# Performance work log

Measured on AMD Instinct MI355X. Metric: run time of the kernel, lower is better.

## Reference

```python
import jax, jax.numpy as jnp
import numpy as np

N, NIN, NOUT = 8192, 512, 512


def setup_inputs() -> dict:
    key = jax.random.key(0)
    k1, k2, k3 = jax.random.split(key, 3)
    H = jax.random.normal(k1, (N, NIN), dtype=jnp.float32)
    adj_matrix = jax.random.uniform(k2, (N, N), dtype=jnp.float32)
    W = jax.random.normal(k3, (NOUT, NIN), dtype=jnp.float32) / np.sqrt(NIN)
    b = jnp.zeros((NOUT,), dtype=jnp.float32)
    return {"H": H, "adj_matrix": adj_matrix, "W": W, "b": b}


def reference(H, adj_matrix, W, b):
    n = adj_matrix.shape[0]
    # adj + I (self-loops)
    A = adj_matrix + jnp.eye(n, dtype=adj_matrix.dtype)
    # column degrees (torch.sum(dim=0))
    deg = jnp.sum(A, axis=0)
    d = deg ** -0.5
    d = jnp.where(jnp.isinf(d), 0.0, d)
    # D^-1/2 A D^-1/2 implemented as elementwise row/col rescale (same math as diag matmuls)
    A = d[:, None] * A * d[None, :]
    # message passing + linear (torch Linear: x @ W.T + b) + tanh
    Hm = A @ H  # [N, nin]
    out = jnp.tanh(Hm @ W.T + b)
    return out
```

## Files before the change

### kernel.cpp

```cpp
#include <hip/hip_runtime.h>
#include <hip/hip_bf16.h>

#define N_NODES 8192
#define N_IN 512
#define N_OUT 512

typedef __bf16 bf16;
typedef __bf16 bf16x4 __attribute__((ext_vector_type(4)));
typedef __bf16 bf16x8 __attribute__((ext_vector_type(8)));
typedef float f32x4 __attribute__((ext_vector_type(4)));

__device__ __forceinline__ void gload16(const void* g, void* l) {
  __builtin_amdgcn_global_load_lds((const __attribute__((address_space(1))) void*)g,
                                   (__attribute__((address_space(3))) void*)l, 16, 0, 0);
}

#define WAITVM(N) asm volatile("s_waitcnt vmcnt(" #N ")" ::: "memory")
#define BAR() do { asm volatile("" ::: "memory"); __builtin_amdgcn_s_barrier(); \
                   asm volatile("" ::: "memory"); } while (0)

__global__ __launch_bounds__(256) void k_colsum_cvt(const float* __restrict__ adj,
                                                    bf16* __restrict__ adjb,
                                                    float* __restrict__ partial) {
  const int tid  = threadIdx.x;
  const int col0 = blockIdx.x * 1024 + tid * 4;
  const int row0 = blockIdx.y * 64;
  float s0 = 0.f, s1 = 0.f, s2 = 0.f, s3 = 0.f;
#pragma unroll 4
  for (int r = 0; r < 64; ++r) {
    float4 v = *reinterpret_cast<const float4*>(adj + (size_t)(row0 + r) * N_NODES + col0);
    s0 += v.x; s1 += v.y; s2 += v.z; s3 += v.w;
    const int dq = row0 + r - col0;
    if ((unsigned)dq < 4u) reinterpret_cast<float*>(&v)[dq] += 1.0f;
    bf16x4 o = { (bf16)v.x, (bf16)v.y, (bf16)v.z, (bf16)v.w };
    *reinterpret_cast<bf16x4*>(adjb + (size_t)(row0 + r) * N_NODES + col0) = o;
  }
  float4 ps = { s0, s1, s2, s3 };
  *reinterpret_cast<float4*>(partial + (size_t)blockIdx.y * N_NODES + col0) = ps;
}

__global__ __launch_bounds__(256) void k_dvec(const float* __restrict__ partial,
                                              float* __restrict__ dv) {
  const int j = blockIdx.x * 256 + threadIdx.x;
  float s = 1.0f;
#pragma unroll 8
  for (int p = 0; p < 128; ++p) s += partial[(size_t)p * N_NODES + j];
  dv[j] = rsqrtf(s);
}

__global__ __launch_bounds__(256) void k_hst(const float* __restrict__ H,
                                             const float* __restrict__ dv,
                                             bf16* __restrict__ Hst) {
  __shared__ float t[64][65];
  const int tid = threadIdx.x;
  const int j0 = blockIdx.x * 64;
  const int k0 = blockIdx.y * 64;
  const int rr = tid >> 4;
  const int cc = (tid & 15) * 4;
#pragma unroll
  for (int p = 0; p < 4; ++p) {
    const int r = p * 16 + rr;
    const float d = dv[j0 + r];
    float4 v = *reinterpret_cast<const float4*>(H + (size_t)(j0 + r) * N_IN + k0 + cc);
    t[r][cc + 0] = v.x * d; t[r][cc + 1] = v.y * d;
    t[r][cc + 2] = v.z * d; t[r][cc + 3] = v.w * d;
  }
  __syncthreads();
#pragma unroll
  for (int p = 0; p < 4; ++p) {
    const int kr = p * 16 + rr;
    bf16x4 o = { (bf16)t[cc + 0][kr], (bf16)t[cc + 1][kr],
                 (bf16)t[cc + 2][kr], (bf16)t[cc + 3][kr] };
    *reinterpret_cast<bf16x4*>(Hst + (size_t)(k0 + kr) * N_NODES + j0 + cc) = o;
  }
}

__global__ __launch_bounds__(256) void k_wcvt(const float* __restrict__ W, bf16* __restrict__ Wb) {
  const int i = (blockIdx.x * 256 + threadIdx.x) * 4;
  float4 v = *reinterpret_cast<const float4*>(W + i);
  bf16x4 o = { (bf16)v.x, (bf16)v.y, (bf16)v.z, (bf16)v.w };
  *reinterpret_cast<bf16x4*>(Wb + i) = o;
}

template<int KDIM, int NSPLIT>
__global__ __launch_bounds__(512, 2) void k_gemm256(
    const bf16* __restrict__ A, const bf16* __restrict__ B, float* __restrict__ P) {
  constexpr int KSEG = KDIM / NSPLIT;
  constexpr int NT = KSEG / 32;
  constexpr int NTN = 2;
  constexpr int NBLK = 32 * NTN * NSPLIT;
  __shared__ __attribute__((aligned(128))) char lds[4 * 32768];

  const int bid = blockIdx.x;
  const int logical = (bid & 7) * (NBLK / 8) + (bid >> 3);
  const int split = logical / (32 * NTN);
  const int rem = logical % (32 * NTN);
  const int bm0 = (rem >> 1) * 256;
  const int bn0 = (rem & 1) * 256;

  const int tid = threadIdx.x;
  const int lane = tid & 63;
  const int wid = tid >> 6;
  const int wr = wid >> 2;
  const int wc = wid & 3;

  const int srow = tid >> 2;
  const int scol = ((tid & 3) ^ ((srow >> 1) & 3)) << 3;
  const size_t a_src = (size_t)(bm0 + srow) * KDIM + (size_t)split * KSEG + scol;
  const size_t b_src = (size_t)(bn0 + srow) * KDIM + (size_t)split * KSEG + scol;

  const int frow = lane & 15;
  const int fk = lane >> 4;
  const int colb = (fk << 4) ^ (((frow >> 1) & 3) << 4);
  const int a_base = (wr * 128 + frow) * 64 + colb;
  const int b_base = 16384 + (wc * 64 + frow) * 64 + colb;

  f32x4 acc[8][4] = {};

  auto stage_full = [&](int t) {
    char* sb = lds + (t & 3) * 32768;
    const bf16* ag = A + a_src + (size_t)t * 32;
    const bf16* bg = B + b_src + (size_t)t * 32;
    gload16(ag,                      sb +         tid * 16);
    gload16(ag + (size_t)128 * KDIM, sb +  8192 + tid * 16);
    gload16(bg,                      sb + 16384 + tid * 16);
    gload16(bg + (size_t)128 * KDIM, sb + 24576 + tid * 16);
  };

  stage_full(0); stage_full(1);
  WAITVM(4);
  BAR();

#pragma unroll 1
  for (int t = 0; t < NT; ++t) {
    const char* lbase = lds + (t & 3) * 32768;
    char* sbase = lds + ((t + 2) & 3) * 32768;
    const bf16* ag = A + a_src + (size_t)(t + 2) * 32;
    const bf16* bg = B + b_src + (size_t)(t + 2) * 32;
    const bool pf = (t + 2 < NT);

    bf16x8 av[8], bv[4];
#pragma unroll
    for (int m = 0; m < 4; ++m)
      av[m] = *reinterpret_cast<const bf16x8*>(lbase + a_base + m * 1024);
#pragma unroll
    for (int n = 0; n < 4; ++n)
      bv[n] = *reinterpret_cast<const bf16x8*>(lbase + b_base + n * 1024);
    if (pf) {
      gload16(ag,                      sbase +        tid * 16);
      gload16(ag + (size_t)128 * KDIM, sbase + 8192 + tid * 16);
    }
    BAR();
    __builtin_amdgcn_s_setprio(1);
#pragma unroll
    for (int m = 0; m < 4; ++m)
#pragma unroll
      for (int n = 0; n < 4; ++n)
        acc[m][n] = __builtin_amdgcn_mfma_f32_16x16x32_bf16(av[m], bv[n], acc[m][n], 0, 0, 0);
    __builtin_amdgcn_s_setprio(0);
    BAR();
#pragma unroll
    for (int m = 4; m < 8; ++m)
      av[m] = *reinterpret_cast<const bf16x8*>(lbase + a_base + m * 1024);
    if (pf) {
      gload16(bg,                      sbase + 16384 + tid * 16);
      gload16(bg + (size_t)128 * KDIM, sbase + 24576 + tid * 16);
    }
    BAR();
    __builtin_amdgcn_s_setprio(1);
#pragma unroll
    for (int m = 4; m < 8; ++m)
#pragma unroll
      for (int n = 0; n < 4; ++n)
        acc[m][n] = __builtin_amdgcn_mfma_f32_16x16x32_bf16(av[m], bv[n], acc[m][n], 0, 0, 0);
    __builtin_amdgcn_s_setprio(0);
    if (pf) WAITVM(4); else WAITVM(0);
    BAR();
  }

#pragma unroll
  for (int m = 0; m < 8; ++m) {
#pragma unroll
    for (int j = 0; j < 4; ++j) {
      const int grow = bm0 + wr * 128 + m * 16 + (lane >> 4) * 4 + j;
      float* prow = P + (size_t)split * ((size_t)N_NODES * N_IN) + (size_t)grow * N_IN;
#pragma unroll
      for (int n = 0; n < 4; ++n) {
        const int gcol = bn0 + wc * 64 + n * 16 + (lane & 15);
        prow[gcol] = acc[m][n][j];
      }
    }
  }
}

template<int KDIM>
__global__ __launch_bounds__(256, 2) void k_gemm(
    const bf16* __restrict__ A, const bf16* __restrict__ B,
    const float* __restrict__ bias, float* __restrict__ outf) {
  constexpr int NT = KDIM / 64;
  constexpr int NBLK = 256;
  __shared__ __attribute__((aligned(128))) char lds[2 * 32768];

  const int bid = blockIdx.x;
  const int logical = (bid & 7) * (NBLK / 8) + (bid >> 3);
  const int bm0 = (logical >> 2) * 128;
  const int bn0 = (logical & 3) * 128;

  const int tid = threadIdx.x;
  const int wid = tid >> 6;
  const int lane = tid & 63;
  const int wr = wid & 1, wc = wid >> 1;

  const int srow = tid >> 3;
  const int scol = ((tid & 7) ^ (srow & 7)) << 3;
  const size_t a_src = (size_t)(bm0 + srow) * KDIM + scol;
  const size_t b_src = (size_t)(bn0 + srow) * KDIM + scol;

  const int frow = lane & 15;
  const int fk = lane >> 4;
  const int swz = (lane & 7) << 4;
  const int a_row_byte = (wr * 64 + frow) * 128;
  const int b_row_byte = 16384 + (wc * 64 + frow) * 128;

  f32x4 acc[4][4] = {};

  auto stage = [&](int t) {
    char* lbase = lds + (t & 1) * 32768;
    const bf16* ag = A + a_src + (size_t)t * 64;
    const bf16* bg = B + b_src + (size_t)t * 64;
#pragma unroll
    for (int ch = 0; ch < 4; ++ch) {
      gload16(ag + (size_t)(ch * 32) * KDIM, lbase + ch * 4096 + wid * 1024);
      gload16(bg + (size_t)(ch * 32) * KDIM, lbase + 16384 + ch * 4096 + wid * 1024);
    }
  };

  auto compute = [&](int t) {
    const char* lbase = lds + (t & 1) * 32768;
#pragma unroll
    for (int kk = 0; kk < 2; ++kk) {
      const int colb = (kk * 64 + fk * 16) ^ swz;
      bf16x8 av[4], bv[4];
#pragma unroll
      for (int m = 0; m < 4; ++m)
        av[m] = *reinterpret_cast<const bf16x8*>(lbase + a_row_byte + m * 2048 + colb);
#pragma unroll
      for (int n = 0; n < 4; ++n)
        bv[n] = *reinterpret_cast<const bf16x8*>(lbase + b_row_byte + n * 2048 + colb);
#pragma unroll
      for (int m = 0; m < 4; ++m)
#pragma unroll
        for (int n = 0; n < 4; ++n)
          acc[m][n] = __builtin_amdgcn_mfma_f32_16x16x32_bf16(av[m], bv[n], acc[m][n], 0, 0, 0);
    }
  };

  stage(0);
#pragma unroll 1
  for (int t = 0; t < NT - 1; ++t) {
    stage(t + 1);
    WAITVM(8);
    BAR();
    compute(t);
    BAR();
  }
  WAITVM(0);
  BAR();
  compute(NT - 1);

#pragma unroll
  for (int m = 0; m < 4; ++m) {
#pragma unroll
    for (int j = 0; j < 4; ++j) {
      const int grow = bm0 + wr * 64 + m * 16 + (lane >> 4) * 4 + j;
      float* orow = outf + (size_t)grow * N_OUT;
#pragma unroll
      for (int n = 0; n < 4; ++n) {
        const int gcol = bn0 + wc * 64 + n * 16 + (lane & 15);
        float v = acc[m][n][j] + bias[gcol];
        v = fminf(fmaxf(v, -15.f), 15.f);
        const float e = __expf(2.f * v);
        orow[gcol] = (e - 1.f) / (e + 1.f);
      }
    }
  }
}

__global__ __launch_bounds__(256) void k_red(const float* __restrict__ P,
                                             const float* __restrict__ dv,
                                             bf16* __restrict__ Hm) {
  const int t = blockIdx.x * 256 + threadIdx.x;
  const int row = t >> 7;
  const int col = (t & 127) << 2;
  const size_t off = (size_t)row * N_IN + col;
  constexpr size_t S = (size_t)N_NODES * N_IN;
  const float d = dv[row];
  const float4 p0 = *reinterpret_cast<const float4*>(P + off);
  const float4 p1 = *reinterpret_cast<const float4*>(P + S + off);
  const float4 p2 = *reinterpret_cast<const float4*>(P + 2 * S + off);
  const float4 p3 = *reinterpret_cast<const float4*>(P + 3 * S + off);
  bf16x4 o = { (bf16)(d * ((p0.x + p1.x) + (p2.x + p3.x))),
               (bf16)(d * ((p0.y + p1.y) + (p2.y + p3.y))),
               (bf16)(d * ((p0.z + p1.z) + (p2.z + p3.z))),
               (bf16)(d * ((p0.w + p1.w) + (p2.w + p3.w))) };
  *reinterpret_cast<bf16x4*>(Hm + off) = o;
}

extern "C" void kernel_launch(void* const* d_in, const int* in_sizes, int n_in,
                              void* d_out, int out_size, void* d_ws, size_t ws_size,
                              hipStream_t stream) {
  const float* H   = (const float*)d_in[0];
  const float* adj = (const float*)d_in[1];
  const float* W   = (const float*)d_in[2];
  const float* b   = (const float*)d_in[3];
  float* out = (float*)d_out;
  char* ws = (char*)d_ws;

  bf16*  adjb = (bf16*)(ws);
  bf16*  Hst  = (bf16*)(ws + 134217728);
  bf16*  Hm   = (bf16*)(ws + 142606336);
  bf16*  Wb   = (bf16*)(ws + 150994944);
  float* part = (float*)(ws + 151519232);
  float* dv   = (float*)(ws + 155713536);
  float* P    = (float*)(ws + 155746304);

  k_colsum_cvt<<<dim3(8, 128), 256, 0, stream>>>(adj, adjb, part);
  k_dvec<<<32, 256, 0, stream>>>(part, dv);
  k_hst<<<dim3(128, 8), 256, 0, stream>>>(H, dv, Hst);
  k_wcvt<<<256, 256, 0, stream>>>(W, Wb);
  k_gemm256<8192, 4><<<256, 512, 0, stream>>>(adjb, Hst, P);
  k_red<<<4096, 256, 0, stream>>>(P, dv, Hm);
  k_gemm<512><<<256, 256, 0, stream>>>(Hm, Wb, b, out);
}
```

Baseline: 212.2 us.

## Deepen K-tile to 64 with four-phase interleaved prefetch in 256x256 GEMM

Restructures the 256x256 bf16 MFMA GEMM main loop to process K in 64-wide tiles with two 64KB LDS buffers instead of four 32-wide buffers. Each tile is split into four MFMA phases with global-to-LDS loads for the next tiles spread across them and fine-grained vmcnt waits. It also switches to an 8-way XOR swizzle over 128-byte rows. The aim is fewer barrier-bound iterations and better overlap of loads with MFMA work. In exchange there are more barriers per iteration, more complex wait counts, and B fragments held in registers across phases.

```diff
diff --git a/kernel.cpp b/kernel.cpp
--- a/kernel.cpp
+++ b/kernel.cpp
@@ -86,10 +86,10 @@
 __global__ __launch_bounds__(512, 2) void k_gemm256(
     const bf16* __restrict__ A, const bf16* __restrict__ B, float* __restrict__ P) {
   constexpr int KSEG = KDIM / NSPLIT;
-  constexpr int NT = KSEG / 32;
+  constexpr int NT = KSEG / 64;
   constexpr int NTN = 2;
   constexpr int NBLK = 32 * NTN * NSPLIT;
-  __shared__ __attribute__((aligned(128))) char lds[4 * 32768];
+  __shared__ __attribute__((aligned(128))) char lds[2 * 65536];
 
   const int bid = blockIdx.x;
   const int logical = (bid & 7) * (NBLK / 8) + (bid >> 3);
@@ -104,79 +104,105 @@
   const int wr = wid >> 2;
   const int wc = wid & 3;
 
-  const int srow = tid >> 2;
-  const int scol = ((tid & 3) ^ ((srow >> 1) & 3)) << 3;
-  const size_t a_src = (size_t)(bm0 + srow) * KDIM + (size_t)split * KSEG + scol;
-  const size_t b_src = (size_t)(bn0 + srow) * KDIM + (size_t)split * KSEG + scol;
+  const int lrow = lane >> 3;
+  const int g_srow = wid * 8 + lrow;
+  const int g_scol = ((lane & 7) ^ lrow) << 3;
+  const size_t koff = (size_t)split * KSEG;
+  const bf16* aP = A + (size_t)(bm0 + g_srow) * KDIM + koff + g_scol;
+  const bf16* bP = B + (size_t)(bn0 + g_srow) * KDIM + koff + g_scol;
+  const int ldst = wid * 1024;
 
   const int frow = lane & 15;
   const int fk = lane >> 4;
-  const int colb = (fk << 4) ^ (((frow >> 1) & 3) << 4);
-  const int a_base = (wr * 128 + frow) * 64 + colb;
-  const int b_base = 16384 + (wc * 64 + frow) * 64 + colb;
+  const int e7 = lane & 7;
+  const int sb0 = ((fk ^ e7) << 4);
+  const int sb1 = (((4 + fk) ^ e7) << 4);
+  const int a_b = (wr * 128 + frow) * 128;
+  const int b_b = 32768 + (wc * 64 + frow) * 128;
 
   f32x4 acc[8][4] = {};
 
-  auto stage_full = [&](int t) {
-    char* sb = lds + (t & 3) * 32768;
-    const bf16* ag = A + a_src + (size_t)t * 32;
-    const bf16* bg = B + b_src + (size_t)t * 32;
-    gload16(ag,                      sb +         tid * 16);
-    gload16(ag + (size_t)128 * KDIM, sb +  8192 + tid * 16);
-    gload16(bg,                      sb + 16384 + tid * 16);
-    gload16(bg + (size_t)128 * KDIM, sb + 24576 + tid * 16);
-  };
-
-  stage_full(0); stage_full(1);
-  WAITVM(4);
+  auto GLA = [&](int kt, int q, int buf) {
+    gload16(aP + (size_t)(q * 64) * KDIM + (size_t)kt * 64,
+            lds + buf * 65536 + q * 8192 + ldst);
+  };
+  auto GLB = [&](int kt, int q, int buf) {
+    gload16(bP + (size_t)(q * 64) * KDIM + (size_t)kt * 64,
+            lds + buf * 65536 + 32768 + q * 8192 + ldst);
+  };
+
+  auto phases = [&](int kt, bool s1, bool s2, bool s3, int f2, int f4) {
+    const char* lb = lds + (kt & 1) * 65536;
+    const int ob = (kt & 1) ^ 1;
+    const int cb = (kt & 1);
+    bf16x8 av[4], bv0[4], bv1[4];
+#pragma unroll
+    for (int m = 0; m < 4; ++m) av[m]  = *(const bf16x8*)(lb + a_b + m * 2048 + sb0);
+#pragma unroll
+    for (int n = 0; n < 4; ++n) bv0[n] = *(const bf16x8*)(lb + b_b + n * 2048 + sb0);
+#pragma unroll
+    for (int n = 0; n < 4; ++n) bv1[n] = *(const bf16x8*)(lb + b_b + n * 2048 + sb1);
+    if (s1) { GLA(kt + 1, 1, ob); GLA(kt + 1, 3, ob); }
+    BAR();
+    __builtin_amdgcn_s_setprio(1);
+#pragma unroll
+    for (int m = 0; m < 4; ++m)
+#pragma unroll
+      for (int n = 0; n < 4; ++n)
+        acc[m][n] = __builtin_amdgcn_mfma_f32_16x16x32_bf16(av[m], bv0[n], acc[m][n], 0, 0, 0);
+    __builtin_amdgcn_s_setprio(0);
+    BAR();
+#pragma unroll
+    for (int m = 0; m < 4; ++m) av[m] = *(const bf16x8*)(lb + a_b + m * 2048 + sb1);
+    if (s2) { GLB(kt + 2, 0, cb); GLB(kt + 2, 1, cb); }
+    BAR();
+    __builtin_amdgcn_s_setprio(1);
+#pragma unroll
+    for (int m = 0; m < 4; ++m)
+#pragma unroll
+      for (int n = 0; n < 4; ++n)
+        acc[m][n] = __builtin_amdgcn_mfma_f32_16x16x32_bf16(av[m], bv1[n], acc[m][n], 0, 0, 0);
+    __builtin_amdgcn_s_setprio(0);
+    if (f2 == 0) WAITVM(10); else if (f2 == 1) WAITVM(8); else WAITVM(0);
+    BAR();
+#pragma unroll
+    for (int m = 0; m < 4; ++m) av[m] = *(const bf16x8*)(lb + a_b + (m + 4) * 2048 + sb0);
+    if (s3) { GLB(kt + 2, 2, cb); GLB(kt + 2, 3, cb); GLA(kt + 2, 0, cb); GLA(kt + 2, 2, cb); }
+    BAR();
+    __builtin_amdgcn_s_setprio(1);
+#pragma unroll
+    for (int m = 0; m < 4; ++m)
+#pragma unroll
+      for (int n = 0; n < 4; ++n)
+        acc[m + 4][n] = __builtin_amdgcn_mfma_f32_16x16x32_bf16(av[m], bv0[n], acc[m + 4][n], 0, 0, 0);
+    __builtin_amdgcn_s_setprio(0);
+    BAR();
+#pragma unroll
+    for (int m = 0; m < 4; ++m) av[m] = *(const bf16x8*)(lb + a_b + (m + 4) * 2048 + sb1);
+    BAR();
+    __builtin_amdgcn_s_setprio(1);
+#pragma unroll
+    for (int m = 0; m < 4; ++m)
+#pragma unroll
+      for (int n = 0; n < 4; ++n)
+        acc[m + 4][n] = __builtin_amdgcn_mfma_f32_16x16x32_bf16(av[m], bv1[n], acc[m + 4][n], 0, 0, 0);
+    __builtin_amdgcn_s_setprio(0);
+    if (f4 == 0) WAITVM(8); else if (f4 == 1) WAITVM(2); else WAITVM(0);
+    BAR();
+  };
+
+  GLA(0, 0, 0); GLA(0, 2, 0); GLB(0, 0, 0); GLB(0, 1, 0); GLB(0, 2, 0); GLB(0, 3, 0);
+  GLA(0, 1, 0); GLA(0, 3, 0);
+  GLB(1, 0, 1); GLB(1, 1, 1);
+  GLB(1, 2, 1); GLB(1, 3, 1); GLA(1, 0, 1); GLA(1, 2, 1);
+  WAITVM(8);
   BAR();
 
 #pragma unroll 1
-  for (int t = 0; t < NT; ++t) {
-    const char* lbase = lds + (t & 3) * 32768;
-    char* sbase = lds + ((t + 2) & 3) * 32768;
-    const bf16* ag = A + a_src + (size_t)(t + 2) * 32;
-    const bf16* bg = B + b_src + (size_t)(t + 2) * 32;
-    const bool pf = (t + 2 < NT);
-
-    bf16x8 av[8], bv[4];
-#pragma unroll
-    for (int m = 0; m < 4; ++m)
-      av[m] = *reinterpret_cast<const bf16x8*>(lbase + a_base + m * 1024);
-#pragma unroll
-    for (int n = 0; n < 4; ++n)
-      bv[n] = *reinterpret_cast<const bf16x8*>(lbase + b_base + n * 1024);
-    if (pf) {
-      gload16(ag,                      sbase +        tid * 16);
-      gload16(ag + (size_t)128 * KDIM, sbase + 8192 + tid * 16);
-    }
-    BAR();
-    __builtin_amdgcn_s_setprio(1);
-#pragma unroll
-    for (int m = 0; m < 4; ++m)
-#pragma unroll
-      for (int n = 0; n < 4; ++n)
-        acc[m][n] = __builtin_amdgcn_mfma_f32_16x16x32_bf16(av[m], bv[n], acc[m][n], 0, 0, 0);
-    __builtin_amdgcn_s_setprio(0);
-    BAR();
-#pragma unroll
-    for (int m = 4; m < 8; ++m)
-      av[m] = *reinterpret_cast<const bf16x8*>(lbase + a_base + m * 1024);
-    if (pf) {
-      gload16(bg,                      sbase + 16384 + tid * 16);
-      gload16(bg + (size_t)128 * KDIM, sbase + 24576 + tid * 16);
-    }
-    BAR();
-    __builtin_amdgcn_s_setprio(1);
-#pragma unroll
-    for (int m = 4; m < 8; ++m)
-#pragma unroll
-      for (int n = 0; n < 4; ++n)
-        acc[m][n] = __builtin_amdgcn_mfma_f32_16x16x32_bf16(av[m], bv[n], acc[m][n], 0, 0, 0);
-    __builtin_amdgcn_s_setprio(0);
-    if (pf) WAITVM(4); else WAITVM(0);
-    BAR();
-  }
+  for (int kt = 0; kt < NT - 2; ++kt)
+    phases(kt, true, true, true, 0, 0);
+  phases(NT - 2, true, false, false, 1, 1);
+  phases(NT - 1, false, false, false, 2, 2);
 
 #pragma unroll
   for (int m = 0; m < 8; ++m) {
```

Result: faster. 206.6 us (-2.6%).

## Replace 256x256 pipelined GEMM with single-buffered 128x128 tile GEMM at higher occupancy

Applied to the files above, without the earlier changes.

The main adjacency GEMM moves from 256x256 tiles, 512 threads and a 4-stage LDS ring with software prefetch to 128x128 tiles, 256 threads and a single 32KB LDS buffer with K-steps of 64. It launches 1024 blocks instead of 256, relying on four blocks per CU to hide memory latency rather than explicit prefetch. The trade is lower data reuse per tile, which means more global traffic, plus full barriers with no load/compute overlap inside a block.

```diff
diff --git a/kernel.cpp b/kernel.cpp
--- a/kernel.cpp
+++ b/kernel.cpp
@@ -83,106 +83,79 @@
 }
 
 template<int KDIM, int NSPLIT>
-__global__ __launch_bounds__(512, 2) void k_gemm256(
+__global__ __launch_bounds__(256, 4) void k_gemm128(
     const bf16* __restrict__ A, const bf16* __restrict__ B, float* __restrict__ P) {
   constexpr int KSEG = KDIM / NSPLIT;
-  constexpr int NT = KSEG / 32;
-  constexpr int NTN = 2;
-  constexpr int NBLK = 32 * NTN * NSPLIT;
-  __shared__ __attribute__((aligned(128))) char lds[4 * 32768];
+  constexpr int NT = KSEG / 64;
+  constexpr int NBLK = 256 * NSPLIT;
+  __shared__ __attribute__((aligned(128))) char lds[32768];
 
   const int bid = blockIdx.x;
-  const int logical = (bid & 7) * (NBLK / 8) + (bid >> 3);
-  const int split = logical / (32 * NTN);
-  const int rem = logical % (32 * NTN);
-  const int bm0 = (rem >> 1) * 256;
-  const int bn0 = (rem & 1) * 256;
+  const int l = (bid & 7) * (NBLK / 8) + (bid >> 3);
+  const int split = l >> 8;
+  const int rem = l & 255;
+  const int bm0 = (rem >> 2) * 128;
+  const int bn0 = (rem & 3) * 128;
 
   const int tid = threadIdx.x;
   const int lane = tid & 63;
   const int wid = tid >> 6;
-  const int wr = wid >> 2;
-  const int wc = wid & 3;
-
-  const int srow = tid >> 2;
-  const int scol = ((tid & 3) ^ ((srow >> 1) & 3)) << 3;
-  const size_t a_src = (size_t)(bm0 + srow) * KDIM + (size_t)split * KSEG + scol;
-  const size_t b_src = (size_t)(bn0 + srow) * KDIM + (size_t)split * KSEG + scol;
+  const int wr = wid & 1, wc = wid >> 1;
+
+  const int srow = tid >> 3;
+  const int sslot = (tid & 7) ^ (srow & 7);
+  const size_t koff = (size_t)split * KSEG;
+  const bf16* aP = A + (size_t)(bm0 + srow) * KDIM + koff + sslot * 8;
+  const bf16* bP = B + (size_t)(bn0 + srow) * KDIM + koff + sslot * 8;
+  const int wuni = wid * 1024;
 
   const int frow = lane & 15;
   const int fk = lane >> 4;
-  const int colb = (fk << 4) ^ (((frow >> 1) & 3) << 4);
-  const int a_base = (wr * 128 + frow) * 64 + colb;
-  const int b_base = 16384 + (wc * 64 + frow) * 64 + colb;
-
-  f32x4 acc[8][4] = {};
-
-  auto stage_full = [&](int t) {
-    char* sb = lds + (t & 3) * 32768;
-    const bf16* ag = A + a_src + (size_t)t * 32;
-    const bf16* bg = B + b_src + (size_t)t * 32;
-    gload16(ag,                      sb +         tid * 16);
-    gload16(ag + (size_t)128 * KDIM, sb +  8192 + tid * 16);
-    gload16(bg,                      sb + 16384 + tid * 16);
-    gload16(bg + (size_t)128 * KDIM, sb + 24576 + tid * 16);
-  };
-
-  stage_full(0); stage_full(1);
-  WAITVM(4);
-  BAR();
+  const int e7 = lane & 7;
+  const int sb0 = ((fk ^ e7) << 4);
+  const int sb1 = (((4 + fk) ^ e7) << 4);
+  const int a_b = (wr * 64 + frow) * 128;
+  const int b_b = 16384 + (wc * 64 + frow) * 128;
+
+  f32x4 acc[4][4] = {};
 
 #pragma unroll 1
   for (int t = 0; t < NT; ++t) {
-    const char* lbase = lds + (t & 3) * 32768;
-    char* sbase = lds + ((t + 2) & 3) * 32768;
-    const bf16* ag = A + a_src + (size_t)(t + 2) * 32;
-    const bf16* bg = B + b_src + (size_t)(t + 2) * 32;
-    const bool pf = (t + 2 < NT);
-
-    bf16x8 av[8], bv[4];
-#pragma unroll
-    for (int m = 0; m < 4; ++m)
-      av[m] = *reinterpret_cast<const bf16x8*>(lbase + a_base + m * 1024);
-#pragma unroll
-    for (int n = 0; n < 4; ++n)
-      bv[n] = *reinterpret_cast<const bf16x8*>(lbase + b_base + n * 1024);
-    if (pf) {
-      gload16(ag,                      sbase +        tid * 16);
-      gload16(ag + (size_t)128 * KDIM, sbase + 8192 + tid * 16);
-    }
-    BAR();
-    __builtin_amdgcn_s_setprio(1);
-#pragma unroll
-    for (int m = 0; m < 4; ++m)
+    const bf16* ag = aP + (size_t)t * 64;
+    const bf16* bg = bP + (size_t)t * 64;
+    gload16(ag,                       lds +         wuni);
+    gload16(ag + (size_t)32 * KDIM,   lds +  4096 + wuni);
+    gload16(ag + (size_t)64 * KDIM,   lds +  8192 + wuni);
+    gload16(ag + (size_t)96 * KDIM,   lds + 12288 + wuni);
+    gload16(bg,                       lds + 16384 + wuni);
+    gload16(bg + (size_t)32 * KDIM,   lds + 20480 + wuni);
+    gload16(bg + (size_t)64 * KDIM,   lds + 24576 + wuni);
+    gload16(bg + (size_t)96 * KDIM,   lds + 28672 + wuni);
+    __syncthreads();
+#pragma unroll
+    for (int kk = 0; kk < 2; ++kk) {
+      const int sb = kk ? sb1 : sb0;
+      bf16x8 av[4], bv[4];
+#pragma unroll
+      for (int m = 0; m < 4; ++m)
+        av[m] = *reinterpret_cast<const bf16x8*>(lds + a_b + m * 2048 + sb);
 #pragma unroll
       for (int n = 0; n < 4; ++n)
-        acc[m][n] = __builtin_amdgcn_mfma_f32_16x16x32_bf16(av[m], bv[n], acc[m][n], 0, 0, 0);
-    __builtin_amdgcn_s_setprio(0);
-    BAR();
-#pragma unroll
-    for (int m = 4; m < 8; ++m)
-      av[m] = *reinterpret_cast<const bf16x8*>(lbase + a_base + m * 1024);
-    if (pf) {
-      gload16(bg,                      sbase + 16384 + tid * 16);
-      gload16(bg + (size_t)128 * KDIM, sbase + 24576 + tid * 16);
-    }
-    BAR();
-    __builtin_amdgcn_s_setprio(1);
-#pragma unroll
-    for (int m = 4; m < 8; ++m)
-#pragma unroll
-      for (int n = 0; n < 4; ++n)
-        acc[m][n] = __builtin_amdgcn_mfma_f32_16x16x32_bf16(av[m], bv[n], acc[m][n], 0, 0, 0);
-    __builtin_amdgcn_s_setprio(0);
-    if (pf) WAITVM(4); else WAITVM(0);
-    BAR();
-  }
-
-#pragma unroll
-  for (int m = 0; m < 8; ++m) {
+        bv[n] = *reinterpret_cast<const bf16x8*>(lds + b_b + n * 2048 + sb);
+#pragma unroll
+      for (int m = 0; m < 4; ++m)
+#pragma unroll
+        for (int n = 0; n < 4; ++n)
+          acc[m][n] = __builtin_amdgcn_mfma_f32_16x16x32_bf16(av[m], bv[n], acc[m][n], 0, 0, 0);
+    }
+    __syncthreads();
+  }
+
+#pragma unroll
+  for (int m = 0; m < 4; ++m) {
 #pragma unroll
     for (int j = 0; j < 4; ++j) {
-      const int grow = bm0 + wr * 128 + m * 16 + (lane >> 4) * 4 + j;
+      const int grow = bm0 + wr * 64 + m * 16 + (lane >> 4) * 4 + j;
       float* prow = P + (size_t)split * ((size_t)N_NODES * N_IN) + (size_t)grow * N_IN;
 #pragma unroll
       for (int n = 0; n < 4; ++n) {
@@ -328,7 +301,7 @@
   k_dvec<<<32, 256, 0, stream>>>(part, dv);
   k_hst<<<dim3(128, 8), 256, 0, stream>>>(H, dv, Hst);
   k_wcvt<<<256, 256, 0, stream>>>(W, Wb);
-  k_gemm256<8192, 4><<<256, 512, 0, stream>>>(adjb, Hst, P);
+  k_gemm128<8192, 4><<<1024, 256, 0, stream>>>(adjb, Hst, P);
   k_red<<<4096, 256, 0, stream>>>(P, dv, Hm);
   k_gemm<512><<<256, 256, 0, stream>>>(Hm, Wb, b, out);
 }
```

After: 237.3 us. 11.8% more time.
